# Kernel optimization log

Hardware: AMD Instinct MI355X
Metric: run time of the kernel (lower is better)

Reference implementation:

```python
import jax, jax.numpy as jnp
import numpy as np

E, K, H, I = 8, 2, 1024, 3584  # num_experts, top_k, hidden, intermediate


def setup_inputs() -> dict:
    key = jax.random.key(0)
    k0, k1, k2, k3, k4 = jax.random.split(key, 5)
    scale = 0.02
    return {
        "hidden_states": jax.random.normal(k0, (2, 1024, H), dtype=jnp.float32),
        "w_gate": jax.random.normal(k1, (E, H), dtype=jnp.float32) * scale,  # gate Linear H->E
        "w1": jax.random.normal(k2, (E, I, H), dtype=jnp.float32) * scale,   # gate proj
        "w3": jax.random.normal(k3, (E, I, H), dtype=jnp.float32) * scale,   # up proj
        "w2": jax.random.normal(k4, (E, H, I), dtype=jnp.float32) * scale,   # down proj
    }


def reference(hidden_states, w_gate, w1, w3, w2):
    B, S, Hd = hidden_states.shape
    x = hidden_states.reshape(-1, Hd)                       # [T, H]
    logits = jnp.einsum('th,eh->te', x, w_gate)             # router logits [T, E]
    probs = jax.nn.softmax(logits, axis=-1)
    topw, topi = jax.lax.top_k(probs, K)                    # [T, K]
    topw = topw / jnp.sum(topw, axis=-1, keepdims=True)     # renormalize=True
    # dense combine weights [T, E] (zero off the top-k)
    comb = jnp.sum(jax.nn.one_hot(topi, E, dtype=x.dtype) * topw[..., None], axis=1)
    # SwiGLU experts (dense reference over all experts; math matches dispatch+combine)
    g = jnp.einsum('th,eih->eti', x, w1)                    # [E, T, I]
    u = jnp.einsum('th,eih->eti', x, w3)
    h = jax.nn.silu(g) * u
    out = jnp.einsum('eti,ehi->eth', h, w2)                 # [E, T, H]
    y = jnp.einsum('te,eth->th', comb, out)                 # weighted combine
    return y.reshape(B, S, Hd)
```

## Files before the change

### kernel.cpp

```cpp
#include <hip/hip_runtime.h>
#include <hip/hip_bf16.h>
#include <stdint.h>

#define NEXP 8
#define HD 1024
#define ID 3584
#define NTOK 2048
#define NSLOT 4096
#define SLOT_PAD 128
#define NSLOT_ALLOC (NSLOT + SLOT_PAD)
#define WN (NEXP * ID * HD)
#define KSPLIT 4
#define KLEN (ID / KSPLIT)

typedef unsigned short u16;
typedef __attribute__((ext_vector_type(8))) short s16x8;
typedef __attribute__((ext_vector_type(4))) short s16x4;
typedef __attribute__((ext_vector_type(4))) float f32x4;

__device__ __forceinline__ u16 f2bf(float f) {
    __hip_bfloat16 h = __float2bfloat16(f);
    union { __hip_bfloat16 h; u16 u; } v; v.h = h; return v.u;
}

__device__ __forceinline__ s16x8 cvt8(f32x4 a, f32x4 b) {
    s16x8 o;
    o[0]=(short)f2bf(a[0]); o[1]=(short)f2bf(a[1]); o[2]=(short)f2bf(a[2]); o[3]=(short)f2bf(a[3]);
    o[4]=(short)f2bf(b[0]); o[5]=(short)f2bf(b[1]); o[6]=(short)f2bf(b[2]); o[7]=(short)f2bf(b[3]);
    return o;
}

__device__ __forceinline__ void glds16(const void* g, void* l) {
    __builtin_amdgcn_global_load_lds((const __attribute__((address_space(1))) unsigned*)g,
                                     (__attribute__((address_space(3))) unsigned*)l, 16, 0, 0);
}

__global__ void init_kernel(int* __restrict__ counts) {
    if (threadIdx.x < 16) counts[threadIdx.x] = 0;
}

__global__ void router_kernel(const float* __restrict__ x, const float* __restrict__ wg,
                              int* __restrict__ topk_idx, float* __restrict__ topk_w,
                              int* __restrict__ counts) {
    int t = blockIdx.x;
    int lane = threadIdx.x;
    const float* xr = x + (size_t)t * HD;
    float acc[NEXP];
#pragma unroll
    for (int e = 0; e < NEXP; ++e) acc[e] = 0.f;
#pragma unroll
    for (int i = 0; i < HD / 256; ++i) {
        int h = i * 256 + lane * 4;
        f32x4 xv = *(const f32x4*)(xr + h);
#pragma unroll
        for (int e = 0; e < NEXP; ++e) {
            f32x4 wv = *(const f32x4*)(wg + e * HD + h);
            acc[e] += xv[0]*wv[0] + xv[1]*wv[1] + xv[2]*wv[2] + xv[3]*wv[3];
        }
    }
#pragma unroll
    for (int e = 0; e < NEXP; ++e) {
#pragma unroll
        for (int s = 32; s > 0; s >>= 1) acc[e] += __shfl_xor(acc[e], s, 64);
    }
    if (lane == 0) {
        int b0 = 0; float l0 = acc[0];
#pragma unroll
        for (int e = 1; e < NEXP; ++e) if (acc[e] > l0) { l0 = acc[e]; b0 = e; }
        int b1 = (b0 == 0) ? 1 : 0; float l1 = acc[b1];
#pragma unroll
        for (int e = 0; e < NEXP; ++e) {
            if (e == b0 || e == b1) continue;
            if (acc[e] > l1) { l1 = acc[e]; b1 = e; }
        }
        float w0 = 1.f / (1.f + expf(l1 - l0));
        float w1 = 1.f - w0;
        topk_idx[2 * t] = b0; topk_idx[2 * t + 1] = b1;
        topk_w[2 * t] = w0;  topk_w[2 * t + 1] = w1;
        atomicAdd(&counts[b0], 1);
        atomicAdd(&counts[b1], 1);
    }
}

__global__ void scan_kernel(const int* __restrict__ counts, int* __restrict__ offsets,
                            int* __restrict__ rows) {
    if (threadIdx.x == 0) {
        int off = 0;
#pragma unroll
        for (int e = 0; e < NEXP; ++e) { offsets[e] = off; off += counts[e]; }
    }
    if (threadIdx.x < SLOT_PAD) rows[NSLOT + threadIdx.x] = 0;
}

__global__ void assign_kernel(const int* __restrict__ topk_idx, const int* __restrict__ offsets,
                              int* __restrict__ counts2, int* __restrict__ rows,
                              int* __restrict__ slot_of) {
    int i = blockIdx.x * 256 + threadIdx.x;
    int e = topk_idx[i];
    int pos = atomicAdd(&counts2[e], 1);
    int slot = offsets[e] + pos;
    rows[slot] = i >> 1;
    slot_of[i] = slot;
}

__global__ __launch_bounds__(256)
void cvt_bf_kernel(const float* __restrict__ src, u16* __restrict__ dst, int n8) {
    int stride = gridDim.x * 256;
    for (int i = blockIdx.x * 256 + threadIdx.x; i < n8; i += stride) {
        f32x4 v0 = ((const f32x4*)src)[2 * i];
        f32x4 v1 = ((const f32x4*)src)[2 * i + 1];
        ((s16x8*)dst)[i] = cvt8(v0, v1);
    }
}

#define G1_BLOCKS (NEXP * (NTOK / 128) * (ID / 128))
#define CVT2_BLOCKS 1024
__global__ __launch_bounds__(256, 2)
void gemm1_kernel(const u16* __restrict__ xbf, const u16* __restrict__ w1bf,
                  const u16* __restrict__ w3bf, const int* __restrict__ counts,
                  const int* __restrict__ offsets, const int* __restrict__ rows,
                  u16* __restrict__ hbuf,
                  const float* __restrict__ w2, u16* __restrict__ w2bf) {
    __shared__ u16 As[128][32];
    __shared__ u16 B1s[128][32];
    __shared__ u16 B3s[128][32];

    if (blockIdx.x >= G1_BLOCKS) {
        const int stride = CVT2_BLOCKS * 256;
        for (int i = (blockIdx.x - G1_BLOCKS) * 256 + threadIdx.x; i < WN / 8; i += stride) {
            f32x4 v0 = ((const f32x4*)w2)[2 * i];
            f32x4 v1 = ((const f32x4*)w2)[2 * i + 1];
            ((s16x8*)w2bf)[i] = cvt8(v0, v1);
        }
        return;
    }

    const int NT = ID / 128;
    int bid = blockIdx.x;
    int e = bid / (16 * NT);
    int rem = bid - e * (16 * NT);
    int mt = rem / NT;
    int nt = rem - mt * NT;
    int n_e = counts[e];
    int m0 = mt * 128;
    if (m0 >= n_e) return;
    int off = offsets[e];
    int n0 = nt * 128;

    int tid = threadIdx.x;
    int lane = tid & 63;
    int wid = tid >> 6;

    int srow = wid * 32 + (lane >> 2);
    int chunk = ((lane & 3) ^ ((srow >> 1) & 3)) * 8;

    int tokA0 = rows[off + m0 + srow];
    int tokA1 = rows[off + m0 + srow + 16];
    const u16* srcA0 = xbf + (size_t)tokA0 * HD + chunk;
    const u16* srcA1 = xbf + (size_t)tokA1 * HD + chunk;
    const u16* srcB1a = w1bf + ((size_t)e * ID + n0 + srow) * HD + chunk;
    const u16* srcB1b = srcB1a + (size_t)16 * HD;
    const u16* srcB3a = w3bf + ((size_t)e * ID + n0 + srow) * HD + chunk;
    const u16* srcB3b = srcB3a + (size_t)16 * HD;

    f32x4 accg[4][4] = {}, accu[4][4] = {};
    int wm = (wid >> 1) * 64, wn = (wid & 1) * 64;
    int lr = lane & 15;
    int k8sw = ((lane >> 4) ^ ((lr >> 1) & 3)) * 8;

    for (int k0 = 0; k0 < HD; k0 += 32) {
        glds16(srcA0 + k0,  &As[wid * 32][0]);
        glds16(srcA1 + k0,  &As[wid * 32 + 16][0]);
        glds16(srcB1a + k0, &B1s[wid * 32][0]);
        glds16(srcB1b + k0, &B1s[wid * 32 + 16][0]);
        glds16(srcB3a + k0, &B3s[wid * 32][0]);
        glds16(srcB3b + k0, &B3s[wid * 32 + 16][0]);
        __syncthreads();
        s16x8 a[4], b1[4], b3[4];
#pragma unroll
        for (int f = 0; f < 4; ++f) {
            a[f]  = *(const s16x8*)&As[wm + f * 16 + lr][k8sw];
            b1[f] = *(const s16x8*)&B1s[wn + f * 16 + lr][k8sw];
            b3[f] = *(const s16x8*)&B3s[wn + f * 16 + lr][k8sw];
        }
#pragma unroll
        for (int fm = 0; fm < 4; ++fm)
#pragma unroll
            for (int fn = 0; fn < 4; ++fn) {
                accg[fm][fn] = __builtin_amdgcn_mfma_f32_16x16x32_bf16(a[fm], b1[fn], accg[fm][fn], 0, 0, 0);
                accu[fm][fn] = __builtin_amdgcn_mfma_f32_16x16x32_bf16(a[fm], b3[fn], accu[fm][fn], 0, 0, 0);
            }
        __syncthreads();
    }

    int lc = lane & 15;
    int lr4 = (lane >> 4) * 4;
#pragma unroll
    for (int fm = 0; fm < 4; ++fm) {
#pragma unroll
        for (int r = 0; r < 4; ++r) {
            int row = wm + fm * 16 + lr4 + r;
            if (m0 + row < n_e) {
                size_t base = (size_t)(off + m0 + row) * ID + n0 + wn;
#pragma unroll
                for (int fn = 0; fn < 4; ++fn) {
                    float g = accg[fm][fn][r];
                    float u = accu[fm][fn][r];
                    float hv = g * u / (1.f + expf(-g));
                    hbuf[base + fn * 16 + lc] = f2bf(hv);
                }
            }
        }
    }
}

__global__ __launch_bounds__(256, 2)
void gemm2_kernel(const u16* __restrict__ hbuf, const u16* __restrict__ w2bf,
                  const int* __restrict__ counts, const int* __restrict__ offsets,
                  float* __restrict__ out2) {
    const int NT = HD / 128;
    int bid = blockIdx.x;
    int e = bid / (16 * NT * KSPLIT);
    int rem = bid - e * (16 * NT * KSPLIT);
    int mt = rem / (NT * KSPLIT);
    int rem2 = rem - mt * (NT * KSPLIT);
    int nt = rem2 / KSPLIT;
    int ks = rem2 - nt * KSPLIT;
    int n_e = counts[e];
    int m0 = mt * 128;
    if (m0 >= n_e) return;
    int off = offsets[e];
    int n0 = nt * 128;
    int kbase = ks * KLEN;

    __shared__ u16 As[128][32];
    __shared__ u16 Bs[128][32];

    int tid = threadIdx.x;
    int lane = tid & 63;
    int wid = tid >> 6;

    int srow = wid * 32 + (lane >> 2);
    int chunk = ((lane & 3) ^ ((srow >> 1) & 3)) * 8;
    const u16* srcA0 = hbuf + (size_t)(off + m0 + srow) * ID + kbase + chunk;
    const u16* srcA1 = srcA0 + (size_t)16 * ID;
    const u16* srcB0 = w2bf + ((size_t)e * HD + n0 + srow) * ID + kbase + chunk;
    const u16* srcB1 = srcB0 + (size_t)16 * ID;

    f32x4 acc[4][4] = {};
    int wm = (wid >> 1) * 64, wn = (wid & 1) * 64;
    int lr = lane & 15;
    int k8sw = ((lane >> 4) ^ ((lr >> 1) & 3)) * 8;

    for (int k0 = 0; k0 < KLEN; k0 += 32) {
        glds16(srcA0 + k0, &As[wid * 32][0]);
        glds16(srcA1 + k0, &As[wid * 32 + 16][0]);
        glds16(srcB0 + k0, &Bs[wid * 32][0]);
        glds16(srcB1 + k0, &Bs[wid * 32 + 16][0]);
        __syncthreads();
        s16x8 a[4], b[4];
#pragma unroll
        for (int f = 0; f < 4; ++f) {
            a[f] = *(const s16x8*)&As[wm + f * 16 + lr][k8sw];
            b[f] = *(const s16x8*)&Bs[wn + f * 16 + lr][k8sw];
        }
#pragma unroll
        for (int fm = 0; fm < 4; ++fm)
#pragma unroll
            for (int fn = 0; fn < 4; ++fn)
                acc[fm][fn] = __builtin_amdgcn_mfma_f32_16x16x32_bf16(a[fm], b[fn], acc[fm][fn], 0, 0, 0);
        __syncthreads();
    }

    float* outp = out2 + (size_t)ks * NSLOT_ALLOC * HD;
    int lc = lane & 15;
    int lr4 = (lane >> 4) * 4;
#pragma unroll
    for (int fm = 0; fm < 4; ++fm) {
#pragma unroll
        for (int r = 0; r < 4; ++r) {
            int row = wm + fm * 16 + lr4 + r;
            if (m0 + row < n_e) {
                float* dst = outp + (size_t)(off + m0 + row) * HD + n0 + wn;
#pragma unroll
                for (int fn = 0; fn < 4; ++fn)
                    dst[fn * 16 + lc] = acc[fm][fn][r];
            }
        }
    }
}

__global__ void combine_kernel(const float* __restrict__ out2, const int* __restrict__ slot_of,
                               const float* __restrict__ topk_w, float* __restrict__ y) {
    int i = blockIdx.x * 256 + threadIdx.x;
    int t = i >> 8;
    int c = i & 255;
    int s0 = slot_of[2 * t], s1 = slot_of[2 * t + 1];
    float w0 = topk_w[2 * t], w1 = topk_w[2 * t + 1];
    f32x4 o = {0.f, 0.f, 0.f, 0.f};
#pragma unroll
    for (int ks = 0; ks < KSPLIT; ++ks) {
        const float* p = out2 + (size_t)ks * NSLOT_ALLOC * HD;
        f32x4 a = ((const f32x4*)(p + (size_t)s0 * HD))[c];
        f32x4 b = ((const f32x4*)(p + (size_t)s1 * HD))[c];
#pragma unroll
        for (int j = 0; j < 4; ++j) o[j] += w0 * a[j] + w1 * b[j];
    }
    ((f32x4*)(y + (size_t)t * HD))[c] = o;
}

extern "C" void kernel_launch(void* const* d_in, const int* in_sizes, int n_in,
                              void* d_out, int out_size, void* d_ws, size_t ws_size,
                              hipStream_t stream) {
    (void)in_sizes; (void)n_in; (void)out_size; (void)ws_size;
    const float* x  = (const float*)d_in[0];
    const float* wg = (const float*)d_in[1];
    const float* w1 = (const float*)d_in[2];
    const float* w3 = (const float*)d_in[3];
    const float* w2 = (const float*)d_in[4];
    float* y = (float*)d_out;

    char* ws = (char*)d_ws;
    int*   counts   = (int*)(ws + 0);
    int*   counts2  = (int*)(ws + 32);
    int*   offsets  = (int*)(ws + 64);
    int*   topk_idx = (int*)(ws + 128);
    float* topk_w   = (float*)(ws + 128 + (size_t)NSLOT * 4);
    int*   rows     = (int*)(ws + 128 + (size_t)NSLOT * 8);
    int*   slot_of  = (int*)(ws + 128 + (size_t)NSLOT * 8 + (size_t)NSLOT_ALLOC * 4);
    size_t off_xbf = 128 + (size_t)NSLOT * 12 + (size_t)NSLOT_ALLOC * 4;
    off_xbf = (off_xbf + 255) & ~(size_t)255;
    u16* xbf = (u16*)(ws + off_xbf);
    size_t off_h = off_xbf + (size_t)NTOK * HD * 2;
    u16* hbuf = (u16*)(ws + off_h);
    size_t off_w1 = off_h + (size_t)NSLOT_ALLOC * ID * 2;
    u16* w1bf = (u16*)(ws + off_w1);
    size_t off_w3 = off_w1 + (size_t)WN * 2;
    u16* w3bf = (u16*)(ws + off_w3);
    size_t off_w2 = off_w3 + (size_t)WN * 2;
    u16* w2bf = (u16*)(ws + off_w2);
    size_t off_o2 = off_w2 + (size_t)WN * 2;
    float* out2 = (float*)(ws + off_o2);

    init_kernel<<<1, 64, 0, stream>>>(counts);
    router_kernel<<<NTOK, 64, 0, stream>>>(x, wg, topk_idx, topk_w, counts);
    scan_kernel<<<1, 128, 0, stream>>>(counts, offsets, rows);
    assign_kernel<<<NSLOT / 256, 256, 0, stream>>>(topk_idx, offsets, counts2, rows, slot_of);
    cvt_bf_kernel<<<2048, 256, 0, stream>>>(x, xbf, NTOK * HD / 8);
    cvt_bf_kernel<<<2048, 256, 0, stream>>>(w1, w1bf, WN / 8);
    cvt_bf_kernel<<<2048, 256, 0, stream>>>(w3, w3bf, WN / 8);
    gemm1_kernel<<<G1_BLOCKS + CVT2_BLOCKS, 256, 0, stream>>>(xbf, w1bf, w3bf, counts, offsets, rows, hbuf, w2, w2bf);
    gemm2_kernel<<<NEXP * (NTOK / 128) * (HD / 128) * KSPLIT, 256, 0, stream>>>(hbuf, w2bf, counts, offsets, out2);
    combine_kernel<<<(NTOK * HD / 4) / 256, 256, 0, stream>>>(out2, slot_of, topk_w, y);
}
```

Measured before the change: 342.0 us.

## Merge bf16 conversion launches and remap GEMM block indices for locality and balance

Folds the three separate fp32-to-bf16 conversion launches into a single grid-stride kernel, saving launch and tail overhead. Reorders gemm1's block-to-tile mapping so consecutive blocks cover groups of 8 weight column tiles across all 16 M-tiles, aiming to reuse those weight tiles in L2. Interleaves experts across gemm2 blocks so early-exiting blocks from lightly loaded experts are spread out, evening the per-expert work across the GPU. The new index math hard-codes the grid shape (28 N-tiles, 8 experts, 16 M-tiles), so it breaks if those constants change.

```diff
diff --git a/kernel.cpp b/kernel.cpp
--- a/kernel.cpp
+++ b/kernel.cpp
@@ -104,12 +104,19 @@
 }
 
 __global__ __launch_bounds__(256)
-void cvt_bf_kernel(const float* __restrict__ src, u16* __restrict__ dst, int n8) {
+void cvt3_kernel(const float* __restrict__ x, u16* __restrict__ xbf,
+                 const float* __restrict__ w1, u16* __restrict__ w1bf,
+                 const float* __restrict__ w3, u16* __restrict__ w3bf) {
+    const int NX = NTOK * HD / 8, NW = WN / 8;
     int stride = gridDim.x * 256;
-    for (int i = blockIdx.x * 256 + threadIdx.x; i < n8; i += stride) {
-        f32x4 v0 = ((const f32x4*)src)[2 * i];
-        f32x4 v1 = ((const f32x4*)src)[2 * i + 1];
-        ((s16x8*)dst)[i] = cvt8(v0, v1);
+    for (int i = blockIdx.x * 256 + threadIdx.x; i < NX + 2 * NW; i += stride) {
+        const float* s; u16* d; int j;
+        if (i < NX)            { s = x;  d = xbf;  j = i; }
+        else if (i < NX + NW)  { s = w1; d = w1bf; j = i - NX; }
+        else                   { s = w3; d = w3bf; j = i - NX - NW; }
+        f32x4 v0 = ((const f32x4*)s)[2 * j];
+        f32x4 v1 = ((const f32x4*)s)[2 * j + 1];
+        ((s16x8*)d)[j] = cvt8(v0, v1);
     }
 }
 
@@ -135,12 +142,14 @@
         return;
     }
 
-    const int NT = ID / 128;
     int bid = blockIdx.x;
-    int e = bid / (16 * NT);
-    int rem = bid - e * (16 * NT);
-    int mt = rem / NT;
-    int nt = rem - mt * NT;
+    int gq = bid >> 7;
+    int rm = bid & 127;
+    int mt = rm >> 3;
+    int g  = gq * 8 + (rm & 7);
+    int e  = g / 28;
+    int nt = g - e * 28;
+
     int n_e = counts[e];
     int m0 = mt * 128;
     if (m0 >= n_e) return;
@@ -204,9 +213,9 @@
                 size_t base = (size_t)(off + m0 + row) * ID + n0 + wn;
 #pragma unroll
                 for (int fn = 0; fn < 4; ++fn) {
-                    float g = accg[fm][fn][r];
+                    float g2 = accg[fm][fn][r];
                     float u = accu[fm][fn][r];
-                    float hv = g * u / (1.f + expf(-g));
+                    float hv = g2 * u / (1.f + expf(-g2));
                     hbuf[base + fn * 16 + lc] = f2bf(hv);
                 }
             }
@@ -218,14 +227,14 @@
 void gemm2_kernel(const u16* __restrict__ hbuf, const u16* __restrict__ w2bf,
                   const int* __restrict__ counts, const int* __restrict__ offsets,
                   float* __restrict__ out2) {
-    const int NT = HD / 128;
     int bid = blockIdx.x;
-    int e = bid / (16 * NT * KSPLIT);
-    int rem = bid - e * (16 * NT * KSPLIT);
-    int mt = rem / (NT * KSPLIT);
-    int rem2 = rem - mt * (NT * KSPLIT);
-    int nt = rem2 / KSPLIT;
-    int ks = rem2 - nt * KSPLIT;
+    int e = bid & 7;
+    int inner = bid >> 3;
+    int mt = inner >> 5;
+    int r2 = inner & 31;
+    int nt = r2 >> 2;
+    int ks = r2 & 3;
+
     int n_e = counts[e];
     int m0 = mt * 128;
     if (m0 >= n_e) return;
@@ -346,9 +355,7 @@
     router_kernel<<<NTOK, 64, 0, stream>>>(x, wg, topk_idx, topk_w, counts);
     scan_kernel<<<1, 128, 0, stream>>>(counts, offsets, rows);
     assign_kernel<<<NSLOT / 256, 256, 0, stream>>>(topk_idx, offsets, counts2, rows, slot_of);
-    cvt_bf_kernel<<<2048, 256, 0, stream>>>(x, xbf, NTOK * HD / 8);
-    cvt_bf_kernel<<<2048, 256, 0, stream>>>(w1, w1bf, WN / 8);
-    cvt_bf_kernel<<<2048, 256, 0, stream>>>(w3, w3bf, WN / 8);
+    cvt3_kernel<<<4096, 256, 0, stream>>>(x, xbf, w1, w1bf, w3, w3bf);
     gemm1_kernel<<<G1_BLOCKS + CVT2_BLOCKS, 256, 0, stream>>>(xbf, w1bf, w3bf, counts, offsets, rows, hbuf, w2, w2bf);
     gemm2_kernel<<<NEXP * (NTOK / 128) * (HD / 128) * KSPLIT, 256, 0, stream>>>(hbuf, w2bf, counts, offsets, out2);
     combine_kernel<<<(NTOK * HD / 4) / 256, 256, 0, stream>>>(out2, slot_of, topk_w, y);
```

New measurement: 345.2 us. Within noise of the previous version (+0.9%).
